# Kernel optimization log

Measured on AMD Instinct MI355X. Metric: run time of the kernel, lower is better.

Reference implementation:

```python
import jax, jax.numpy as jnp
import numpy as np

B, S, F, V, E, H = 128, 256, 4, 1024, 512, 1024
SCALE = 0.05


def setup_inputs() -> dict:
    key = jax.random.key(0)
    ks = jax.random.split(key, 8)
    return {
        "x": jax.random.randint(ks[0], (B, S, F), 0, V),
        "emb": jax.random.normal(ks[1], (F, V, E), dtype=jnp.float32) * SCALE,
        "proj_w": jax.random.normal(ks[2], (E, E), dtype=jnp.float32) * SCALE,
        "proj_b": jnp.zeros((E,), dtype=jnp.float32),
        "W_ih0": jax.random.normal(ks[3], (4 * H, E), dtype=jnp.float32) * SCALE,
        "W_hh0": jax.random.normal(ks[4], (4 * H, H), dtype=jnp.float32) * SCALE,
        "b_ih0": jnp.zeros((4 * H,), dtype=jnp.float32),
        "b_hh0": jnp.zeros((4 * H,), dtype=jnp.float32),
        "W_ih1": jax.random.normal(ks[5], (4 * H, H), dtype=jnp.float32) * SCALE,
        "W_hh1": jax.random.normal(ks[6], (4 * H, H), dtype=jnp.float32) * SCALE,
        "b_ih1": jnp.zeros((4 * H,), dtype=jnp.float32),
        "b_hh1": jnp.zeros((4 * H,), dtype=jnp.float32),
    }


def _lstm_cell(x_t, h, c, W_ih, W_hh, b_ih, b_hh):
    # PyTorch gate layout: [i, f, g, o] along the 4H axis.
    gates = x_t @ W_ih.T + b_ih + h @ W_hh.T + b_hh  # [B, 4H]
    i_pre, f_pre, g_pre, o_pre = jnp.split(gates, 4, axis=-1)
    c_new = jax.nn.sigmoid(f_pre) * c + jax.nn.sigmoid(i_pre) * jnp.tanh(g_pre)
    h_new = jax.nn.sigmoid(o_pre) * jnp.tanh(c_new)
    return h_new, c_new


def reference(x, emb, proj_w, proj_b,
              W_ih0, W_hh0, b_ih0, b_hh0,
              W_ih1, W_hh1, b_ih1, b_hh1):
    # Sum of per-feature embedding lookups: emb[f][x[:, :, f]]  -> [B, S, E]
    emb_sum = jnp.sum(
        jax.vmap(lambda table, idx: table[idx], in_axes=(0, 2))(emb, x), axis=0
    )
    x_in = emb_sum @ proj_w.T + proj_b  # input_proj (Linear)
    xs = jnp.swapaxes(x_in, 0, 1)  # [S, B, E] for scan over time

    z = jnp.zeros((x.shape[0], H), dtype=x_in.dtype)

    def step(carry, x_t):
        h0, c0, h1, c1 = carry
        h0, c0 = _lstm_cell(x_t, h0, c0, W_ih0, W_hh0, b_ih0, b_hh0)
        h1, c1 = _lstm_cell(h0, h1, c1, W_ih1, W_hh1, b_ih1, b_hh1)
        return (h0, c0, h1, c1), h1

    _, h1_seq = jax.lax.scan(step, (z, z, z, z), xs)  # [S, B, H]
    return jnp.swapaxes(h1_seq, 0, 1)  # [B, S, H]
```

## Files before the change

kernel.cpp:

```cpp
#include <hip/hip_runtime.h>
#include <hip/hip_bf16.h>

#define Bb    128
#define Ss    256
#define Ff    4
#define Vv    1024
#define Ee    512
#define Hh    1024
#define FourH 4096
#define Mrows (Bb * Ss)
#define NBLK  192

typedef _Float16 f16;
typedef __attribute__((ext_vector_type(8))) _Float16 half8;
typedef __attribute__((ext_vector_type(4))) float f32x4;

__global__ void cvt_f16_kernel(const float* __restrict__ s, f16* __restrict__ d, int n) {
    int i = blockIdx.x * blockDim.x + threadIdx.x;
    int stride = gridDim.x * blockDim.x;
    for (; i < n; i += stride) d[i] = (f16)s[i];
}

__global__ void bias_combine_kernel(const float* __restrict__ a, const float* __restrict__ b,
                                    const float* __restrict__ c, const float* __restrict__ d,
                                    float* __restrict__ o0, float* __restrict__ o1) {
    int i = blockIdx.x * blockDim.x + threadIdx.x;
    if (i < FourH) o0[i] = a[i] + b[i];
    else if (i < 2 * FourH) { int j = i - FourH; o1[j] = c[j] + d[j]; }
}

__global__ void emb_kernel(const int* __restrict__ x, const float* __restrict__ emb,
                           f16* __restrict__ out) {
    int r = blockIdx.x;
    int t = threadIdx.x;
    int b = r / Ss, s = r % Ss;
    const int* xr = x + (size_t)r * Ff;
    const float* e0 = emb + (size_t)xr[0] * Ee;
    const float* e1 = emb + (size_t)(Vv + xr[1]) * Ee;
    const float* e2 = emb + (size_t)(2 * Vv + xr[2]) * Ee;
    const float* e3 = emb + (size_t)(3 * Vv + xr[3]) * Ee;
    f16* orow = out + (size_t)(s * Bb + b) * Ee;
    for (int e = t; e < Ee; e += 256) orow[e] = (f16)(e0[e] + e1[e] + e2[e] + e3[e]);
}

#define BM 128
#define BN 128
#define BK 32
#define LDP 40

__global__ __launch_bounds__(256) void gemm_bt_kernel(
    const f16* __restrict__ A, const f16* __restrict__ Bw,
    const float* __restrict__ bias, f16* __restrict__ C,
    int M, int N, int K)
{
    __shared__ f16 As[BM * LDP];
    __shared__ f16 Bs[BN * LDP];
    int tid  = threadIdx.x;
    int n0   = blockIdx.x * BN;
    int m0   = blockIdx.y * BM;
    int w    = tid >> 6, lane = tid & 63;
    int wm   = (w >> 1) * 64, wn = (w & 1) * 64;
    int lrow = lane & 15, koff = lane >> 4;

    f32x4 acc[4][4] = {};

    for (int kb = 0; kb < K; kb += BK) {
        __syncthreads();
        #pragma unroll
        for (int h = 0; h < 2; ++h) {
            int ch  = tid + h * 256;
            int row = ch >> 2;
            int cc  = (ch & 3) * 8;
            *reinterpret_cast<uint4*>(&As[row * LDP + cc]) =
                *reinterpret_cast<const uint4*>(A + (size_t)(m0 + row) * K + kb + cc);
            *reinterpret_cast<uint4*>(&Bs[row * LDP + cc]) =
                *reinterpret_cast<const uint4*>(Bw + (size_t)(n0 + row) * K + kb + cc);
        }
        __syncthreads();
        half8 af[4], bf[4];
        #pragma unroll
        for (int mt = 0; mt < 4; ++mt)
            af[mt] = *reinterpret_cast<const half8*>(&As[(wm + mt * 16 + lrow) * LDP + koff * 8]);
        #pragma unroll
        for (int nt = 0; nt < 4; ++nt)
            bf[nt] = *reinterpret_cast<const half8*>(&Bs[(wn + nt * 16 + lrow) * LDP + koff * 8]);
        #pragma unroll
        for (int mt = 0; mt < 4; ++mt)
            #pragma unroll
            for (int nt = 0; nt < 4; ++nt)
                acc[mt][nt] = __builtin_amdgcn_mfma_f32_16x16x32_f16(af[mt], bf[nt], acc[mt][nt], 0, 0, 0);
    }

    #pragma unroll
    for (int mt = 0; mt < 4; ++mt)
        #pragma unroll
        for (int nt = 0; nt < 4; ++nt) {
            int col = n0 + wn + nt * 16 + lrow;
            float bv = bias[col];
            #pragma unroll
            for (int r = 0; r < 4; ++r) {
                int rowg = m0 + wm + mt * 16 + koff * 4 + r;
                C[(size_t)rowg * N + col] = (f16)(acc[mt][nt][r] + bv);
            }
        }
}

__device__ __forceinline__ void gload_lds16(const void* g, void* l) {
    __builtin_amdgcn_global_load_lds((const __attribute__((address_space(1))) void*)g,
                                     (__attribute__((address_space(3))) void*)l, 16, 0, 0);
}

__device__ __forceinline__ void gst_cc(void* p, unsigned v) {
    asm volatile("global_store_dword %0, %1, off sc0 sc1" :: "v"(p), "v"(v) : "memory");
}

__device__ __forceinline__ float f16lo(unsigned u) {
    return (float)__builtin_bit_cast(f16, (unsigned short)(u & 0xffffu));
}
__device__ __forceinline__ float f16hi(unsigned u) {
    return (float)__builtin_bit_cast(f16, (unsigned short)(u >> 16));
}

__device__ __forceinline__ unsigned aload(unsigned* p) {
    return __hip_atomic_load(p, __ATOMIC_RELAXED, __HIP_MEMORY_SCOPE_AGENT);
}

__device__ __forceinline__ float sigm(float v) { return 1.f / (1.f + __expf(-v)); }

__global__ __launch_bounds__(512, 2) __attribute__((amdgpu_waves_per_eu(2, 2)))
void scan_kernel(
    const f16* __restrict__ gx0,
    int t_begin, int t_end,
    const f16* __restrict__ wih1, const f16* __restrict__ whh0,
    const f16* __restrict__ whh1, const float* __restrict__ bias1,
    f16* __restrict__ h0r,
    f16* __restrict__ h1r,
    float* __restrict__ c0, float* __restrict__ c1,
    float* __restrict__ out, unsigned* __restrict__ bar)
{
    __shared__ __align__(1024) char smem[131072];
    float* ep = (float*)smem;

    const int tid  = threadIdx.x;
    const int wg   = blockIdx.x;
    const int lane = tid & 63;
    const int w    = tid >> 6;
    const int lrow = lane & 15, koff = lane >> 4;
    const unsigned swz   = (unsigned)((lane & 7) << 4);
    const unsigned e0s   = ((unsigned)(koff * 16)) ^ swz;
    const unsigned e1s   = ((unsigned)(64 + koff * 16)) ^ swz;
    const unsigned lane16 = (unsigned)(lane << 4);
    const size_t HSLOT = (size_t)Bb * Hh;

    if (wg < 64) {
        const int rowg = wg >> 5, ug = wg & 31;
        const int np = w & 3, kh = w >> 2;
        const int u0 = ug * 32;
        const size_t growb = (size_t)rowg * 64;
        const int cw = np * 32 + lrow;

        unsigned* arr0 = bar + (0 + rowg) * 32;
        unsigned* rel0 = bar + (2 + rowg) * 32;
        unsigned* rel1 = bar + (6 + rowg) * 32;

        half8 wreg[16][2];
        #pragma unroll
        for (int kc = 0; kc < 16; ++kc)
            #pragma unroll
            for (int nt = 0; nt < 2; ++nt) {
                int c = cw + nt * 16;
                wreg[kc][nt] = *(const half8*)(whh0
                    + (size_t)((c >> 5) * Hh + u0 + (c & 31)) * Hh
                    + kh * 512 + kc * 32 + koff * 8);
            }

        float creg[2][2];
        #pragma unroll
        for (int q = 0; q < 2; ++q) {
            int p = tid + q * 512, row = p >> 4, up = p & 15;
            float2 cc = *(const float2*)&c0[(growb + row) * Hh + u0 + 2 * up];
            creg[q][0] = cc.x; creg[q][1] = cc.y;
        }

        for (int i = t_begin; i < t_end; ++i) {
            if (i < 256) {
                const f16* hp = h0r + (size_t)((unsigned)((i - 1) & 7)) * HSLOT;
                f16*       hw = h0r + (size_t)(i & 7) * HSLOT;
                const f16* gx = gx0 + (size_t)(i - t_begin) * (Bb * FourH);
                const char* hb = (const char*)hp + growb * 2048;

                unsigned gxu[2][4];
                #pragma unroll
                for (int q = 0; q < 2; ++q) {
                    int p = tid + q * 512, row = p >> 4, up = p & 15;
                    const unsigned* gr = (const unsigned*)(gx + (growb + row) * FourH + u0) + up;
                    gxu[q][0] = gr[0];
                    gxu[q][1] = gr[512];
                    gxu[q][2] = gr[1024];
                    gxu[q][3] = gr[1536];
                }

                #pragma unroll
                for (int t = 0; t < 16; ++t) {
                    int row  = w * 8 + (t >> 1);
                    int half = t & 1;
                    gload_lds16(hb + (size_t)row * 2048 + half * 1024
                                   + (lane16 ^ ((unsigned)((row & 7) << 4))),
                                smem + row * 2048 + half * 1024);
                }

                asm volatile("s_waitcnt vmcnt(0)" ::: "memory");
                __syncthreads();

                f32x4 acc[4][2] = {};
                #pragma unroll
                for (int kc = 0; kc < 16; ++kc) {
                    unsigned off = (unsigned)(kh * 1024 + (kc >> 1) * 128)
                                 + ((kc & 1) ? e1s : e0s);
                    half8 a[4];
                    #pragma unroll
                    for (int mt = 0; mt < 4; ++mt)
                        a[mt] = *(const half8*)(smem + (mt * 16 + lrow) * 2048 + off);
                    #pragma unroll
                    for (int mt = 0; mt < 4; ++mt) {
                        acc[mt][0] = __builtin_amdgcn_mfma_f32_16x16x32_f16(a[mt], wreg[kc][0], acc[mt][0], 0, 0, 0);
                        acc[mt][1] = __builtin_amdgcn_mfma_f32_16x16x32_f16(a[mt], wreg[kc][1], acc[mt][1], 0, 0, 0);
                    }
                }
                __syncthreads();
                #pragma unroll
                for (int mt = 0; mt < 4; ++mt)
                    #pragma unroll
                    for (int nt = 0; nt < 2; ++nt) {
                        int c = cw + nt * 16;
                        int rowb = mt * 16 + koff * 4;
                        #pragma unroll
                        for (int r = 0; r < 4; ++r)
                            ep[(kh * 64 + rowb + r) * 128 + c] = acc[mt][nt][r];
                    }
                if (tid == 0) {
                    while ((int)aload(rel1) < i - 6) __builtin_amdgcn_s_sleep(2);
                }
                __syncthreads();
                #pragma unroll
                for (int q = 0; q < 2; ++q) {
                    int p = tid + q * 512, row = p >> 4, up = p & 15, uu = 2 * up;
                    float2 iP = *(const float2*)&ep[row * 128 + uu];
                    float2 iQ = *(const float2*)&ep[(64 + row) * 128 + uu];
                    float2 fP = *(const float2*)&ep[row * 128 + 32 + uu];
                    float2 fQ = *(const float2*)&ep[(64 + row) * 128 + 32 + uu];
                    float2 gP = *(const float2*)&ep[row * 128 + 64 + uu];
                    float2 gQ = *(const float2*)&ep[(64 + row) * 128 + 64 + uu];
                    float2 oP = *(const float2*)&ep[row * 128 + 96 + uu];
                    float2 oQ = *(const float2*)&ep[(64 + row) * 128 + 96 + uu];
                    float ip0 = iP.x + iQ.x + f16lo(gxu[q][0]);
                    float ip1 = iP.y + iQ.y + f16hi(gxu[q][0]);
                    float fp0 = fP.x + fQ.x + f16lo(gxu[q][1]);
                    float fp1 = fP.y + fQ.y + f16hi(gxu[q][1]);
                    float gp0 = gP.x + gQ.x + f16lo(gxu[q][2]);
                    float gp1 = gP.y + gQ.y + f16hi(gxu[q][2]);
                    float op0 = oP.x + oQ.x + f16lo(gxu[q][3]);
                    float op1 = oP.y + oQ.y + f16hi(gxu[q][3]);
                    float cn0 = sigm(fp0) * creg[q][0] + sigm(ip0) * tanhf(gp0);
                    float cn1 = sigm(fp1) * creg[q][1] + sigm(ip1) * tanhf(gp1);
                    creg[q][0] = cn0; creg[q][1] = cn1;
                    f16 hA = (f16)(sigm(op0) * tanhf(cn0));
                    f16 hB = (f16)(sigm(op1) * tanhf(cn1));
                    unsigned hv = (unsigned)__builtin_bit_cast(unsigned short, hA)
                                | ((unsigned)__builtin_bit_cast(unsigned short, hB) << 16);
                    gst_cc((void*)(hw + (growb + row) * Hh + u0 + uu), hv);
                }
            }
            asm volatile("s_waitcnt vmcnt(0)" ::: "memory");
            __syncthreads();
            if (tid == 0) {
                unsigned a = atomicAdd(arr0, 1u);
                unsigned gen = a >> 5;
                if ((a & 31u) == 31u) atomicAdd(rel0, 1u);
                while (aload(rel0) < gen + 1u) __builtin_amdgcn_s_sleep(2);
                if ((i & 7) == 0)
                    __builtin_amdgcn_fence(__ATOMIC_ACQUIRE, "agent");
            }
            __syncthreads();
        }
        #pragma unroll
        for (int q = 0; q < 2; ++q) {
            int p = tid + q * 512, row = p >> 4, up = p & 15;
            *(float2*)&c0[(growb + row) * Hh + u0 + 2 * up] = make_float2(creg[q][0], creg[q][1]);
        }
    } else {
        const int wgl = wg - 64;
        const int rowg = wgl >> 6, ug = wgl & 63;
        const int kq = w;
        const int u0 = ug * 16;
        const size_t growb = (size_t)rowg * 64;
        const int l7 = lane & 7;

        unsigned* arr1 = bar + (4 + rowg) * 32;
        unsigned* rel1 = bar + (6 + rowg) * 32;
        unsigned* rel0 = bar + (2 + rowg) * 32;

        const f16* wbase = (kq < 4) ? wih1 : whh1;
        half8 wreg[8][4];
        #pragma unroll
        for (int kc = 0; kc < 8; ++kc)
            #pragma unroll
            for (int nt = 0; nt < 4; ++nt)
                wreg[kc][nt] = *(const half8*)(wbase
                    + (size_t)(nt * Hh + u0 + lrow) * Hh
                    + (kq & 3) * 256 + kc * 32 + koff * 8);

        const int erow = tid >> 3, eup = tid & 7, euu = 2 * eup;
        float crg0, crg1;
        { float2 cc = *(const float2*)&c1[(growb + erow) * Hh + u0 + euu];
          crg0 = cc.x; crg1 = cc.y; }
        float2 bI = *(const float2*)&bias1[u0 + euu];
        float2 bF = *(const float2*)&bias1[Hh + u0 + euu];
        float2 bG = *(const float2*)&bias1[2 * Hh + u0 + euu];
        float2 bO = *(const float2*)&bias1[3 * Hh + u0 + euu];

        const unsigned wb = (unsigned)kq * 16384u;
        const int r2 = lane >> 5;
        const int chs0 = lane & 31;

        #define STG(rb_, bo_) { \
            _Pragma("unroll") \
            for (int t = 0; t < 8; ++t) { \
                int rl = (rb_) + t * 2 + r2; \
                gload_lds16(src + (size_t)rl * 2048 \
                                + ((unsigned)((chs0 ^ (rl & 7)) << 4)), \
                            smem + wb + (bo_) + (unsigned)(t * 1024)); \
            } }
        #define CMT(mt_, bo_) { \
            _Pragma("unroll") \
            for (int kc = 0; kc < 8; ++kc) { \
                half8 a = *(const half8*)(smem + wb + (bo_) \
                            + (unsigned)(lrow * 512) \
                            + ((unsigned)(((kc * 4 + koff) ^ l7) << 4))); \
                acc[mt_][0] = __builtin_amdgcn_mfma_f32_16x16x32_f16(a, wreg[kc][0], acc[mt_][0], 0, 0, 0); \
                acc[mt_][1] = __builtin_amdgcn_mfma_f32_16x16x32_f16(a, wreg[kc][1], acc[mt_][1], 0, 0, 0); \
                acc[mt_][2] = __builtin_amdgcn_mfma_f32_16x16x32_f16(a, wreg[kc][2], acc[mt_][2], 0, 0, 0); \
                acc[mt_][3] = __builtin_amdgcn_mfma_f32_16x16x32_f16(a, wreg[kc][3], acc[mt_][3], 0, 0, 0); \
            } }

        for (int i = t_begin; i < t_end; ++i) {
            int t1 = i - 1;
            if (t1 >= 0) {
                if (tid == 0) {
                    while ((int)aload(rel0) < i) __builtin_amdgcn_s_sleep(2);
                    if ((i & 7) == 0)
                        __builtin_amdgcn_fence(__ATOMIC_ACQUIRE, "agent");
                }
                __syncthreads();

                const f16* a0 = h0r + (size_t)(t1 & 7) * HSLOT;
                const f16* a1 = h1r + (size_t)((unsigned)((t1 - 1) & 7)) * HSLOT;
                f16*       hw = h1r + (size_t)(t1 & 7) * HSLOT;
                const char* src = ((kq < 4) ? (const char*)a0 : (const char*)a1)
                                + growb * 2048 + (size_t)(kq & 3) * 512;

                f32x4 acc[4][4] = {};
                STG(0, 0u)
                STG(16, 8192u)
                asm volatile("s_waitcnt vmcnt(8)" ::: "memory");
                CMT(0, 0u)
                asm volatile("s_waitcnt lgkmcnt(0)" ::: "memory");
                STG(32, 0u)
                asm volatile("s_waitcnt vmcnt(8)" ::: "memory");
                CMT(1, 8192u)
                asm volatile("s_waitcnt lgkmcnt(0)" ::: "memory");
                STG(48, 8192u)
                asm volatile("s_waitcnt vmcnt(8)" ::: "memory");
                CMT(2, 0u)
                asm volatile("s_waitcnt vmcnt(0)" ::: "memory");
                CMT(3, 8192u)

                #pragma unroll
                for (int mt = 0; mt < 4; ++mt)
                    #pragma unroll
                    for (int nt = 0; nt < 4; ++nt) {
                        int c = nt * 16 + lrow;
                        #pragma unroll
                        for (int r = 0; r < 4; ++r) {
                            int row = mt * 16 + koff * 4 + r;
                            int sw  = (row ^ (row >> 2)) & 3;
                            *(float*)(smem + wb + (unsigned)(row * 256)
                                      + (unsigned)((c ^ (sw << 4)) * 4)) = acc[mt][nt][r];
                        }
                    }
                __syncthreads();
                {
                    int sw = (erow ^ (erow >> 2)) & 3;
                    const char* rbase = smem + (unsigned)(erow * 256);
                    float s0x = bI.x, s0y = bI.y, s1x = bF.x, s1y = bF.y;
                    float s2x = bG.x, s2y = bG.y, s3x = bO.x, s3y = bO.y;
                    #pragma unroll
                    for (int k8 = 0; k8 < 8; ++k8) {
                        const char* base = rbase + (unsigned)k8 * 16384u;
                        float2 v0 = *(const float2*)(base + (unsigned)((( 0 + euu) ^ (sw << 4)) * 4));
                        float2 v1 = *(const float2*)(base + (unsigned)(((16 + euu) ^ (sw << 4)) * 4));
                        float2 v2 = *(const float2*)(base + (unsigned)(((32 + euu) ^ (sw << 4)) * 4));
                        float2 v3 = *(const float2*)(base + (unsigned)(((48 + euu) ^ (sw << 4)) * 4));
                        s0x += v0.x; s0y += v0.y; s1x += v1.x; s1y += v1.y;
                        s2x += v2.x; s2y += v2.y; s3x += v3.x; s3y += v3.y;
                    }
                    float cn0 = sigm(s1x) * crg0 + sigm(s0x) * tanhf(s2x); crg0 = cn0;
                    float cn1 = sigm(s1y) * crg1 + sigm(s0y) * tanhf(s2y); crg1 = cn1;
                    float hn0 = sigm(s3x) * tanhf(cn0);
                    float hn1 = sigm(s3y) * tanhf(cn1);
                    unsigned hv = (unsigned)__builtin_bit_cast(unsigned short, (f16)hn0)
                                | ((unsigned)__builtin_bit_cast(unsigned short, (f16)hn1) << 16);
                    gst_cc((void*)(hw + (growb + erow) * Hh + u0 + euu), hv);
                    *(float2*)&out[(growb + erow) * (size_t)(Ss * Hh)
                                   + (size_t)t1 * Hh + u0 + euu] = make_float2(hn0, hn1);
                }
            }
            asm volatile("s_waitcnt vmcnt(0)" ::: "memory");
            __syncthreads();
            if (tid == 0) {
                unsigned a = atomicAdd(arr1, 1u);
                unsigned gen = a >> 6;
                if ((a & 63u) == 63u) atomicAdd(rel1, 1u);
                while (aload(rel1) < gen + 1u) __builtin_amdgcn_s_sleep(2);
            }
            __syncthreads();
        }
        *(float2*)&c1[(growb + erow) * Hh + u0 + euu] = make_float2(crg0, crg1);
        #undef STG
        #undef CMT
    }
}

extern "C" void kernel_launch(void* const* d_in, const int* in_sizes, int n_in,
                              void* d_out, int out_size, void* d_ws, size_t ws_size,
                              hipStream_t stream) {
    const int*   x      = (const int*)  d_in[0];
    const float* emb    = (const float*)d_in[1];
    const float* proj_w = (const float*)d_in[2];
    const float* proj_b = (const float*)d_in[3];
    const float* W_ih0  = (const float*)d_in[4];
    const float* W_hh0  = (const float*)d_in[5];
    const float* b_ih0  = (const float*)d_in[6];
    const float* b_hh0  = (const float*)d_in[7];
    const float* W_ih1  = (const float*)d_in[8];
    const float* W_hh1  = (const float*)d_in[9];
    const float* b_ih1  = (const float*)d_in[10];
    const float* b_hh1  = (const float*)d_in[11];
    float* out = (float*)d_out;

    char* ws = (char*)d_ws;
    f16* emb_sum = (f16*)(ws);
    f16* x_in    = (f16*)(ws + 33554432ull);
    f16* gates   = (f16*)(ws + 67108864ull);
    char* wp     = ws + 201326592ull;
    f16* pw_f   = (f16*)wp; wp += (size_t)Ee * Ee * 2;
    f16* wih0_f = (f16*)wp; wp += (size_t)FourH * Ee * 2;
    f16* whh0_f = (f16*)wp; wp += (size_t)FourH * Hh * 2;
    f16* wih1_f = (f16*)wp; wp += (size_t)FourH * Hh * 2;
    f16* whh1_f = (f16*)wp; wp += (size_t)FourH * Hh * 2;
    float* bias0 = (float*)wp; wp += FourH * 4;
    float* bias1 = (float*)wp; wp += FourH * 4;
    char* zbase = wp;
    f16*   h0r = (f16*)wp;   wp += 8ull * Bb * Hh * 2;
    f16*   h1r = (f16*)wp;   wp += 8ull * Bb * Hh * 2;
    float* c0  = (float*)wp; wp += (size_t)Bb * Hh * 4;
    float* c1  = (float*)wp; wp += (size_t)Bb * Hh * 4;
    unsigned* bar = (unsigned*)wp; wp += 4096;
    size_t zbytes = (size_t)(wp - zbase);

    cvt_f16_kernel<<<512, 256, 0, stream>>>(proj_w, pw_f,   Ee * Ee);
    cvt_f16_kernel<<<512, 256, 0, stream>>>(W_ih0,  wih0_f, FourH * Ee);
    cvt_f16_kernel<<<512, 256, 0, stream>>>(W_hh0,  whh0_f, FourH * Hh);
    cvt_f16_kernel<<<512, 256, 0, stream>>>(W_ih1,  wih1_f, FourH * Hh);
    cvt_f16_kernel<<<512, 256, 0, stream>>>(W_hh1,  whh1_f, FourH * Hh);
    bias_combine_kernel<<<32, 256, 0, stream>>>(b_ih0, b_hh0, b_ih1, b_hh1, bias0, bias1);
    hipMemsetAsync(zbase, 0, zbytes, stream);

    emb_kernel<<<Mrows, 256, 0, stream>>>(x, emb, emb_sum);
    gemm_bt_kernel<<<dim3(Ee / BN, Mrows / BM), 256, 0, stream>>>(
        emb_sum, pw_f, proj_b, x_in, Mrows, Ee, Ee);

    const int CM = Mrows / 2;

    for (int half = 0; half < 2; ++half) {
        gemm_bt_kernel<<<dim3(FourH / BN, CM / BM), 256, 0, stream>>>(
            x_in + (size_t)half * CM * Ee, wih0_f, bias0, gates, CM, FourH, Ee);
        int tb = half * 128;
        int te = (half == 0) ? 128 : 257;
        const f16* gxp = gates;
        void* args[] = { (void*)&gxp, (void*)&tb, (void*)&te,
                         (void*)&wih1_f, (void*)&whh0_f, (void*)&whh1_f, (void*)&bias1,
                         (void*)&h0r, (void*)&h1r,
                         (void*)&c0, (void*)&c1, (void*)&out, (void*)&bar };
        hipLaunchCooperativeKernel((const void*)scan_kernel, dim3(NBLK), dim3(512),
                                   args, 0, stream);
    }
}
```

Measured before the change: 2.794 ms.

## Replace arrive/release barriers with monotonic counters polled per wave

Replaces the two-phase grid barrier (arrival counter plus release counter that a single thread spins on) with monotonic arrival counters. Each wave polls the counter it depends on: layer-0 blocks wait on their own row group's arrivals, and layer-1 waves wait on layer-0 or layer-1 arrivals depending on which input half they read. Producers now only increment the counter and never wait at the end of a step. This removes the full barrier round trip and block-wide waits, so layer-1 waves reading h0 can start before layer-1 peers finish. In exchange every wave polls the same global atomics, which adds contention, and the acquire fence now runs only every 8 steps, which makes memory visibility reasoning more fragile.

```diff
diff --git a/kernel.cpp b/kernel.cpp
--- a/kernel.cpp
+++ b/kernel.cpp
@@ -125,6 +125,10 @@
     return __hip_atomic_load(p, __ATOMIC_RELAXED, __HIP_MEMORY_SCOPE_AGENT);
 }
 
+__device__ __forceinline__ void wave_gate(unsigned* ctr, int target) {
+    while ((int)aload(ctr) < target) __builtin_amdgcn_s_sleep(2);
+}
+
 __device__ __forceinline__ float sigm(float v) { return 1.f / (1.f + __expf(-v)); }
 
 __global__ __launch_bounds__(512, 2) __attribute__((amdgpu_waves_per_eu(2, 2)))
@@ -160,8 +164,7 @@
         const int cw = np * 32 + lrow;
 
         unsigned* arr0 = bar + (0 + rowg) * 32;
-        unsigned* rel0 = bar + (2 + rowg) * 32;
-        unsigned* rel1 = bar + (6 + rowg) * 32;
+        unsigned* arr1 = bar + (2 + rowg) * 32;
 
         half8 wreg[16][2];
         #pragma unroll
@@ -184,6 +187,12 @@
 
         for (int i = t_begin; i < t_end; ++i) {
             if (i < 256) {
+                wave_gate(arr0, 32 * i);
+                if ((i & 7) == 0) {
+                    __syncthreads();
+                    if (tid == 0) __builtin_amdgcn_fence(__ATOMIC_ACQUIRE, "agent");
+                    __syncthreads();
+                }
                 const f16* hp = h0r + (size_t)((unsigned)((i - 1) & 7)) * HSLOT;
                 f16*       hw = h0r + (size_t)(i & 7) * HSLOT;
                 const f16* gx = gx0 + (size_t)(i - t_begin) * (Bb * FourH);
@@ -238,9 +247,7 @@
                         for (int r = 0; r < 4; ++r)
                             ep[(kh * 64 + rowb + r) * 128 + c] = acc[mt][nt][r];
                     }
-                if (tid == 0) {
-                    while ((int)aload(rel1) < i - 6) __builtin_amdgcn_s_sleep(2);
-                }
+                wave_gate(arr1, 64 * (i - 6));
                 __syncthreads();
                 #pragma unroll
                 for (int q = 0; q < 2; ++q) {
@@ -273,15 +280,7 @@
             }
             asm volatile("s_waitcnt vmcnt(0)" ::: "memory");
             __syncthreads();
-            if (tid == 0) {
-                unsigned a = atomicAdd(arr0, 1u);
-                unsigned gen = a >> 5;
-                if ((a & 31u) == 31u) atomicAdd(rel0, 1u);
-                while (aload(rel0) < gen + 1u) __builtin_amdgcn_s_sleep(2);
-                if ((i & 7) == 0)
-                    __builtin_amdgcn_fence(__ATOMIC_ACQUIRE, "agent");
-            }
-            __syncthreads();
+            if (tid == 0) atomicAdd(arr0, 1u);
         }
         #pragma unroll
         for (int q = 0; q < 2; ++q) {
@@ -296,9 +295,8 @@
         const size_t growb = (size_t)rowg * 64;
         const int l7 = lane & 7;
 
-        unsigned* arr1 = bar + (4 + rowg) * 32;
-        unsigned* rel1 = bar + (6 + rowg) * 32;
-        unsigned* rel0 = bar + (2 + rowg) * 32;
+        unsigned* arr0 = bar + (0 + rowg) * 32;
+        unsigned* arr1 = bar + (2 + rowg) * 32;
 
         const f16* wbase = (kq < 4) ? wih1 : whh1;
         half8 wreg[8][4];
@@ -346,12 +344,13 @@
         for (int i = t_begin; i < t_end; ++i) {
             int t1 = i - 1;
             if (t1 >= 0) {
-                if (tid == 0) {
-                    while ((int)aload(rel0) < i) __builtin_amdgcn_s_sleep(2);
-                    if ((i & 7) == 0)
-                        __builtin_amdgcn_fence(__ATOMIC_ACQUIRE, "agent");
-                }
-                __syncthreads();
+                if (kq < 4) wave_gate(arr0, 32 * i);
+                else        wave_gate(arr1, 64 * i);
+                if ((i & 7) == 0) {
+                    __syncthreads();
+                    if (tid == 0) __builtin_amdgcn_fence(__ATOMIC_ACQUIRE, "agent");
+                    __syncthreads();
+                }
 
                 const f16* a0 = h0r + (size_t)(t1 & 7) * HSLOT;
                 const f16* a1 = h1r + (size_t)((unsigned)((t1 - 1) & 7)) * HSLOT;
@@ -417,13 +416,7 @@
             }
             asm volatile("s_waitcnt vmcnt(0)" ::: "memory");
             __syncthreads();
-            if (tid == 0) {
-                unsigned a = atomicAdd(arr1, 1u);
-                unsigned gen = a >> 6;
-                if ((a & 63u) == 63u) atomicAdd(rel1, 1u);
-                while (aload(rel1) < gen + 1u) __builtin_amdgcn_s_sleep(2);
-            }
-            __syncthreads();
+            if (tid == 0) atomicAdd(arr1, 1u);
         }
         *(float2*)&c1[(growb + erow) * Hh + u0 + euu] = make_float2(crg0, crg1);
         #undef STG
```

Measured after the change: 3.162 ms. +13.2%, slower.
